# Kernel tuning notes

Measured on AMD Instinct MI355X. Metric: run time of the kernel, lower is better.

The kernel has to match this reference:

```python
import jax, jax.numpy as jnp
import numpy as np

HEADS = 16
DIM_HEAD = 64
LN_EPS = 1e-3  # keras LayerNormalization default


def setup_inputs() -> dict:
    key = jax.random.key(0)
    ks = jax.random.split(key, 4)
    B, N, D = 8, 512, 1024
    inner = HEADS * DIM_HEAD  # 1024
    return {
        "x": jax.random.normal(ks[0], (B, N, D), dtype=jnp.float32),
        "w_qkv": jax.random.normal(ks[1], (D, 3 * inner), dtype=jnp.float32) * (D ** -0.5),
        "reattn_w": jax.random.normal(ks[2], (HEADS, HEADS), dtype=jnp.float32),
        "ln_gamma": jnp.ones((HEADS,), dtype=jnp.float32),
        "ln_beta": jnp.zeros((HEADS,), dtype=jnp.float32),
        "w_out": jax.random.normal(ks[3], (inner, D), dtype=jnp.float32) * (inner ** -0.5),
        "b_out": jnp.zeros((D,), dtype=jnp.float32),
    }


def reference(x, w_qkv, reattn_w, ln_gamma, ln_beta, w_out, b_out):
    B, N, D = x.shape
    H, dh = HEADS, DIM_HEAD
    scale = dh ** -0.5

    qkv = x @ w_qkv  # [B, N, 3*H*dh]
    q, k, v = jnp.split(qkv, 3, axis=-1)
    # b n (h d) -> b h n d
    to_heads = lambda t: t.reshape(B, N, H, dh).transpose(0, 2, 1, 3)
    q, k, v = to_heads(q), to_heads(k), to_heads(v)

    dots = jnp.einsum("bhid,bhjd->bhij", q, k) * scale  # [B, H, N, N]
    attn = jax.nn.softmax(dots, axis=-1)

    # re-attention: mix across heads
    attn = jnp.einsum("bhij,hg->bgij", attn, reattn_w)

    # LayerNorm over the head axis (axis=1), keras default eps
    mean = jnp.mean(attn, axis=1, keepdims=True)
    var = jnp.var(attn, axis=1, keepdims=True)
    attn = (attn - mean) * jax.lax.rsqrt(var + LN_EPS)
    attn = attn * ln_gamma[None, :, None, None] + ln_beta[None, :, None, None]

    out = jnp.einsum("bhij,bhjd->bhid", attn, v)  # [B, H, N, dh]
    out = out.transpose(0, 2, 1, 3).reshape(B, N, H * dh)  # b h n d -> b n (h d)
    return out @ w_out + b_out
```

## Files before the change

kernel.cpp:

```cpp
#include <hip/hip_runtime.h>
#include <math.h>

#define BB 8
#define NN 512
#define DD 1024
#define HH 16
#define DH 64
#define INNER 1024
#define QKV3 3072
#define PSTR (NN * NN + 64)

typedef __attribute__((ext_vector_type(8))) short short8;
typedef __attribute__((ext_vector_type(4))) float f32x4;

#define AS1 __attribute__((address_space(1)))
#define AS3 __attribute__((address_space(3)))

__device__ __forceinline__ float4 ld4(const float* p) { return *(const float4*)p; }

__device__ __forceinline__ unsigned short f2bf(float f) {
    unsigned u = __float_as_uint(f);
    return (unsigned short)((u + 0x7fffu + ((u >> 16) & 1u)) >> 16);
}
__device__ __forceinline__ float bf2f(unsigned short u) {
    return __uint_as_float(((unsigned)u) << 16);
}

__global__ void preprocess(const float* __restrict__ x, unsigned short* __restrict__ xb,
                           const float* __restrict__ wq, unsigned short* __restrict__ wqT,
                           const float* __restrict__ wo, unsigned short* __restrict__ woT) {
    __shared__ float t[32][33];
    const int tid = threadIdx.x;
    const int bx = blockIdx.x;
    if (bx < 4096) {
        size_t i = ((size_t)bx * 256 + tid) * 4;
        float4 v = ld4(x + i);
        ushort4 o;
        o.x = f2bf(v.x); o.y = f2bf(v.y); o.z = f2bf(v.z); o.w = f2bf(v.w);
        *(ushort4*)(xb + i) = o;
        return;
    }
    const float* in; unsigned short* out; int K, N, n0, k0;
    if (bx < 7168) {
        const int bb = bx - 4096;
        in = wq; out = wqT; K = DD; N = QKV3;
        n0 = (bb % 96) * 32; k0 = (bb / 96) * 32;
    } else {
        const int bb = bx - 7168;
        in = wo; out = woT; K = INNER; N = INNER;
        n0 = (bb & 31) * 32; k0 = (bb >> 5) * 32;
    }
    const int tx = tid & 31, ty = tid >> 5;
#pragma unroll
    for (int l = 0; l < 4; ++l)
        t[ty + 8 * l][tx] = in[(size_t)(k0 + ty + 8 * l) * N + n0 + tx];
    __syncthreads();
#pragma unroll
    for (int l = 0; l < 4; ++l)
        out[(size_t)(n0 + ty + 8 * l) * K + k0 + tx] = f2bf(t[tx][ty + 8 * l]);
}

__device__ __forceinline__ void stage128(const unsigned short* __restrict__ A,
                                         const unsigned short* __restrict__ Bt,
                                         int K, int bm, int bn, int kt,
                                         short* sb, int w, int l) {
#pragma unroll
    for (int t = 0; t < 2; ++t) {
        const int q = w * 2 + t;
        const int li = q * 512 + l * 8;
        const int row = li >> 5, kc = li & 31;
        __builtin_amdgcn_global_load_lds(
            (const AS1 void*)(A + (size_t)(bm + row) * K + kt * 32 + kc),
            (AS3 void*)(sb + q * 512), 16, 0, 0);
        __builtin_amdgcn_global_load_lds(
            (const AS1 void*)(Bt + (size_t)(bn + row) * K + kt * 32 + kc),
            (AS3 void*)(sb + 4096 + q * 512), 16, 0, 0);
    }
}

__global__ __launch_bounds__(256) void gemm_bf16(
    const unsigned short* __restrict__ A, const unsigned short* __restrict__ Bt,
    float* __restrict__ C, const float* __restrict__ bias, int M, int N, int K) {
    __shared__ __align__(16) short lds_[2 * 8192];
    const int tid = threadIdx.x;
    const int w = tid >> 6, l = tid & 63;
    const int bm = blockIdx.y * 128, bn = blockIdx.x * 128;
    const int wm = (w >> 1) * 64, wn = (w & 1) * 64;
    const int lrow = l & 15, lq = l >> 4;
    const int NT = K >> 5;

    f32x4 acc[4][4];
#pragma unroll
    for (int i = 0; i < 4; ++i)
#pragma unroll
        for (int j = 0; j < 4; ++j) acc[i][j] = (f32x4){0.f, 0.f, 0.f, 0.f};

    stage128(A, Bt, K, bm, bn, 0, lds_, w, l);
    asm volatile("s_waitcnt vmcnt(0)" ::: "memory");
    __builtin_amdgcn_s_barrier();

    for (int t = 0; t < NT; ++t) {
        const int s = t & 1;
        if (t + 1 < NT)
            stage128(A, Bt, K, bm, bn, t + 1, lds_ + (s ^ 1) * 8192, w, l);
        const short* As_ = lds_ + s * 8192;
        const short* Bs_ = As_ + 4096;
        short8 a[4], b[4];
#pragma unroll
        for (int i = 0; i < 4; ++i)
            a[i] = *(const short8*)(As_ + (wm + i * 16 + lrow) * 32 + lq * 8);
#pragma unroll
        for (int j = 0; j < 4; ++j)
            b[j] = *(const short8*)(Bs_ + (wn + j * 16 + lrow) * 32 + lq * 8);

        asm volatile("s_waitcnt lgkmcnt(0)" ::: "memory");
        __builtin_amdgcn_sched_barrier(0);

        __builtin_amdgcn_s_setprio(1);
#pragma unroll
        for (int i = 0; i < 4; ++i)
#pragma unroll
            for (int j = 0; j < 4; ++j)
                acc[i][j] = __builtin_amdgcn_mfma_f32_16x16x32_bf16(a[i], b[j], acc[i][j], 0, 0, 0);
        __builtin_amdgcn_s_setprio(0);

        asm volatile("s_waitcnt vmcnt(0)" ::: "memory");
        __builtin_amdgcn_s_barrier();
    }

#pragma unroll
    for (int i = 0; i < 4; ++i)
#pragma unroll
        for (int j = 0; j < 4; ++j) {
            const int col = bn + wn + j * 16 + lrow;
            const float bv = bias ? bias[col] : 0.f;
#pragma unroll
            for (int r = 0; r < 4; ++r) {
                const int row = bm + wm + i * 16 + lq * 4 + r;
                C[(size_t)row * N + col] = acc[i][j][r] + bv;
            }
        }
}

__device__ __forceinline__ void stage_st(const unsigned short* __restrict__ G, int K,
                                         int row0, int kt, short* dst_half,
                                         int w, int l) {
    const int grow = row0 + w * 16 + (l >> 2);
    const int gcol = kt * 32 + (((l & 3) * 8) ^ ((l & 32) ? 16 : 0));
    __builtin_amdgcn_global_load_lds(
        (const AS1 void*)(G + (size_t)grow * K + gcol),
        (AS3 void*)(dst_half + w * 512), 16, 0, 0);
}

__global__ __launch_bounds__(512, 4) void gemm256_bf(
    const unsigned short* __restrict__ A, const unsigned short* __restrict__ Bt,
    unsigned short* __restrict__ C, int M, int N, int K) {
    __shared__ __align__(16) short lds_[2 * 12288];
    const int tid = threadIdx.x;
    const int w = tid >> 6, l = tid & 63;
    const int wmi = w >> 1, wni = w & 1;
    const int lrow = l & 15, lq = l >> 4;
    const int bm = blockIdx.y * 256, bn = blockIdx.x * 128;
    const int NT = K >> 5;

    const int aoff = lrow * 32 + ((lq * 8) ^ ((lrow & 8) ? 16 : 0));

    f32x4 acc[4][4];
#pragma unroll
    for (int i = 0; i < 4; ++i)
#pragma unroll
        for (int j = 0; j < 4; ++j) acc[i][j] = (f32x4){0.f, 0.f, 0.f, 0.f};

    stage_st(A,  K, bm,       0, lds_ + 0,    w, l);
    stage_st(A,  K, bm + 128, 0, lds_ + 4096, w, l);
    stage_st(Bt, K, bn,       0, lds_ + 8192, w, l);
    asm volatile("s_waitcnt vmcnt(0)" ::: "memory");
    __builtin_amdgcn_s_barrier();

    for (int t = 0; t < NT; ++t) {
        const int s = t & 1;
        if (t + 1 < NT) {
            short* nb = lds_ + (s ^ 1) * 12288;
            stage_st(A,  K, bm,       t + 1, nb,        w, l);
            stage_st(A,  K, bm + 128, t + 1, nb + 4096, w, l);
            stage_st(Bt, K, bn,       t + 1, nb + 8192, w, l);
        }
        const short* cb = lds_ + s * 12288;
        short8 a[4], b[4];
#pragma unroll
        for (int i = 0; i < 4; ++i)
            a[i] = *(const short8*)(cb + (wmi * 4 + i) * 512 + aoff);
#pragma unroll
        for (int j = 0; j < 4; ++j)
            b[j] = *(const short8*)(cb + 8192 + (wni * 4 + j) * 512 + aoff);

        asm volatile("s_waitcnt lgkmcnt(0)" ::: "memory");
        __builtin_amdgcn_sched_barrier(0);

        __builtin_amdgcn_s_setprio(1);
#pragma unroll
        for (int i = 0; i < 4; ++i)
#pragma unroll
            for (int j = 0; j < 4; ++j)
                acc[i][j] = __builtin_amdgcn_mfma_f32_16x16x32_bf16(a[i], b[j], acc[i][j], 0, 0, 0);
        __builtin_amdgcn_s_setprio(0);

        asm volatile("s_waitcnt vmcnt(0)" ::: "memory");
        __builtin_amdgcn_s_barrier();
    }

#pragma unroll
    for (int i = 0; i < 4; ++i)
#pragma unroll
        for (int j = 0; j < 4; ++j) {
            const int col = bn + wni * 64 + j * 16 + lrow;
#pragma unroll
            for (int r = 0; r < 4; ++r) {
                const int row = bm + wmi * 64 + i * 16 + lq * 4 + r;
                C[(size_t)row * N + col] = f2bf(acc[i][j][r]);
            }
        }
}

__global__ __launch_bounds__(256) void scores_tv(
    const unsigned short* __restrict__ qkvb, unsigned short* __restrict__ attnb,
    unsigned short* __restrict__ vT, float* __restrict__ lsum2) {
    __shared__ unsigned short sh[256 * 64 + 4 * 16 * 68];
    const int bx = blockIdx.x;
    const int tid = threadIdx.x;

    if (bx >= 2048) {
        const int t = bx - 2048;
        const int j0 = (t & 15) * 32;
        const int d0 = ((t >> 4) & 1) * 32;
        const int bh = t >> 5;
        const int h = bh & 15, b = bh >> 4;
        unsigned short (*tt)[33] = (unsigned short(*)[33])sh;
        const int tx = tid & 31, ty = tid >> 5;
        const unsigned short* src = qkvb + (size_t)(b * NN) * QKV3 + 2 * INNER + h * DH;
#pragma unroll
        for (int k = 0; k < 4; ++k)
            tt[ty + 8 * k][tx] = src[(size_t)(j0 + ty + 8 * k) * QKV3 + d0 + tx];
        __syncthreads();
        unsigned short* dst = vT + (size_t)bh * DH * NN;
#pragma unroll
        for (int k = 0; k < 4; ++k)
            dst[(size_t)(d0 + ty + 8 * k) * NN + j0 + tx] = tt[tx][ty + 8 * k];
        return;
    }

    unsigned short* Ks = sh;
    unsigned short* obuf = sh + 16384;
    const int bh = bx & 127;
    const int h = bh & 15, b = bh >> 4;
    const int jh = (bx >> 7) & 1;
    const int w = tid >> 6, l = tid & 63;
    const int i0 = (bx >> 8) * 64 + w * 16;
    const int lrow = l & 15, lq = l >> 4;

    const unsigned short* kbase =
        qkvb + (size_t)(b * NN + jh * 256) * QKV3 + INNER + h * DH;
#pragma unroll
    for (int i = 0; i < 8; ++i) {
        const int r = (w * 8 + i) * 8 + (l >> 3);
        const int c = (l & 7) ^ (r & 7);
        __builtin_amdgcn_global_load_lds(
            (const AS1 void*)(kbase + (size_t)r * QKV3 + c * 8),
            (AS3 void*)(Ks + (w * 8 + i) * 512), 16, 0, 0);
    }

    const unsigned short* qb = qkvb + (size_t)(b * NN) * QKV3 + h * DH + lq * 8;
    const short8 qf0 = *(const short8*)(qb + (size_t)(i0 + lrow) * QKV3);
    const short8 qf1 = *(const short8*)(qb + (size_t)(i0 + lrow) * QKV3 + 32);

    asm volatile("s_waitcnt vmcnt(0)" ::: "memory");
    __syncthreads();

    unsigned short* obase = attnb + (size_t)bh * PSTR + (size_t)i0 * NN + jh * 256;
    unsigned short* ob = obuf + (w * 16) * 68;
    const int sw = lrow & 7;
    float lacc = 0.f;
#pragma unroll
    for (int jt = 0; jt < 16; ++jt) {
        const int R = jt * 16 + lrow;
        const short8 kf0 = *(const short8*)(Ks + R * 64 + ((lq ^ sw) * 8));
        const short8 kf1 = *(const short8*)(Ks + R * 64 + (((4 + lq) ^ sw) * 8));
        f32x4 acc = (f32x4){0.f, 0.f, 0.f, 0.f};
        acc = __builtin_amdgcn_mfma_f32_16x16x32_bf16(kf0, qf0, acc, 0, 0, 0);
        acc = __builtin_amdgcn_mfma_f32_16x16x32_bf16(kf1, qf1, acc, 0, 0, 0);
        float e0 = __expf(acc[0] * 0.125f);
        float e1 = __expf(acc[1] * 0.125f);
        float e2 = __expf(acc[2] * 0.125f);
        float e3 = __expf(acc[3] * 0.125f);
        lacc += (e0 + e1) + (e2 + e3);
        ushort4 o;
        o.x = f2bf(e0); o.y = f2bf(e1); o.z = f2bf(e2); o.w = f2bf(e3);
        *(ushort4*)(ob + lrow * 68 + (jt & 3) * 16 + lq * 4) = o;
        if ((jt & 3) == 3) {
            const int jb = (jt >> 2) * 64;
#pragma unroll
            for (int q = 0; q < 4; ++q) {
                const int rr = q * 4 + (l >> 4);
                const int cc = l & 15;
                *(ushort4*)(obase + (size_t)rr * NN + jb + cc * 4) =
                    *(const ushort4*)(ob + rr * 68 + cc * 4);
            }
        }
    }
    lacc += __shfl_xor(lacc, 16, 64);
    lacc += __shfl_xor(lacc, 32, 64);
    if (lq == 0)
        lsum2[(size_t)jh * BB * HH * NN + (size_t)bh * NN + i0 + lrow] = lacc;
}

__global__ __launch_bounds__(512) void reattn_pv(
    const unsigned short* __restrict__ attnb, const unsigned short* __restrict__ vT,
    const float* __restrict__ lsum2, const float* __restrict__ rw,
    const float* __restrict__ gamma, const float* __restrict__ beta,
    unsigned short* __restrict__ outhb) {
    __shared__ unsigned short Ash[16 * 16 * 64];
    __shared__ float wsh[16][16];
    __shared__ float linv[16][16];
    __shared__ float gsh[16], bsh[16];

    const int b = blockIdx.x >> 5;
    const int i0 = (blockIdx.x & 31) * 16;
    const int tid = threadIdx.x;
    const int w = tid >> 6, l = tid & 63;
    const int lrow = l & 15, lq = l >> 4;

    if (tid < 256) {
        ((float*)wsh)[tid] = rw[tid];
        const int h = tid >> 4, i = tid & 15;
        const float s =
            lsum2[(size_t)(b * HH + h) * NN + i0 + i] +
            lsum2[(size_t)BB * HH * NN + (size_t)(b * HH + h) * NN + i0 + i];
        linv[h][i] = 1.0f / s;
    }
    if (tid < 16) { gsh[tid] = gamma[tid]; bsh[tid] = beta[tid]; }

    const int ri = w * 2 + (l >> 5);
    const int rj = (l & 31) * 2;
    const unsigned short* ebase =
        attnb + (size_t)(b * HH) * PSTR + (size_t)(i0 + ri) * NN + rj;

    f32x4 acc[2][4];
#pragma unroll
    for (int gg = 0; gg < 2; ++gg)
#pragma unroll
        for (int dt = 0; dt < 4; ++dt) acc[gg][dt] = (f32x4){0.f, 0.f, 0.f, 0.f};

    unsigned e[16];
#pragma unroll
    for (int h = 0; h < 16; ++h)
        e[h] = *(const unsigned*)(ebase + (size_t)h * PSTR);

    __syncthreads();

    const int g0 = w * 2;
    const int cch = rj >> 3;
    const int csw = ((cch ^ (ri & 7)) << 3) + (rj & 7);

    for (int jt = 0; jt < 8; ++jt) {
        float e0[16], e1[16];
#pragma unroll
        for (int h = 0; h < 16; ++h) {
            const float li = linv[h][ri];
            e0[h] = bf2f((unsigned short)(e[h] & 0xffffu)) * li;
            e1[h] = bf2f((unsigned short)(e[h] >> 16)) * li;
        }
        float m0[16], m1[16];
        float mean0 = 0.f, mean1 = 0.f;
#pragma unroll
        for (int g = 0; g < 16; ++g) {
            float s0 = 0.f, s1 = 0.f;
#pragma unroll
            for (int h = 0; h < 16; ++h) {
                const float wg = wsh[h][g];
                s0 += e0[h] * wg; s1 += e1[h] * wg;
            }
            m0[g] = s0; m1[g] = s1;
            mean0 += s0; mean1 += s1;
        }
        mean0 *= 0.0625f; mean1 *= 0.0625f;
        float va0 = 0.f, va1 = 0.f;
#pragma unroll
        for (int g = 0; g < 16; ++g) {
            const float d0 = m0[g] - mean0, d1 = m1[g] - mean1;
            va0 += d0 * d0; va1 += d1 * d1;
        }
        const float ri0 = rsqrtf(va0 * 0.0625f + 1e-3f);
        const float ri1 = rsqrtf(va1 * 0.0625f + 1e-3f);
#pragma unroll
        for (int g = 0; g < 16; ++g) {
            const unsigned short a0 = f2bf((m0[g] - mean0) * ri0 * gsh[g] + bsh[g]);
            const unsigned short a1 = f2bf((m1[g] - mean1) * ri1 * gsh[g] + bsh[g]);
            *(unsigned*)(&Ash[(g * 16 + ri) * 64 + csw]) = ((unsigned)a1 << 16) | (unsigned)a0;
        }
        __syncthreads();

        if (jt < 7) {
#pragma unroll
            for (int h = 0; h < 16; ++h)
                e[h] = *(const unsigned*)(ebase + (size_t)h * PSTR + (jt + 1) * 64);
        }
        const int j0 = jt * 64;
#pragma unroll
        for (int gg = 0; gg < 2; ++gg) {
            const int g = g0 + gg;
            const unsigned short* vb = vT + (size_t)(b * HH + g) * DH * NN;
#pragma unroll
            for (int kc = 0; kc < 2; ++kc) {
                const int cc = kc * 4 + lq;
                const short8 pf = *(const short8*)(
                    &Ash[(g * 16 + lrow) * 64 + ((cc ^ (lrow & 7)) << 3)]);
#pragma unroll
                for (int dt = 0; dt < 4; ++dt) {
                    const short8 vf = *(const short8*)(
                        vb + (size_t)(dt * 16 + lrow) * NN + j0 + kc * 32 + lq * 8);
                    acc[gg][dt] = __builtin_amdgcn_mfma_f32_16x16x32_bf16(
                        vf, pf, acc[gg][dt], 0, 0, 0);
                }
            }
        }
        __syncthreads();
    }

#pragma unroll
    for (int gg = 0; gg < 2; ++gg) {
        const int g = g0 + gg;
        unsigned short* orow = outhb +
            (size_t)(b * NN + i0 + lrow) * INNER + g * DH + lq * 4;
#pragma unroll
        for (int dt = 0; dt < 4; ++dt) {
            ushort4 o;
            o.x = f2bf(acc[gg][dt][0]); o.y = f2bf(acc[gg][dt][1]);
            o.z = f2bf(acc[gg][dt][2]); o.w = f2bf(acc[gg][dt][3]);
            *(ushort4*)(orow + dt * 16) = o;
        }
    }
}

extern "C" void kernel_launch(void* const* d_in, const int* in_sizes, int n_in,
                              void* d_out, int out_size, void* d_ws, size_t ws_size,
                              hipStream_t stream) {
    const float* x        = (const float*)d_in[0];
    const float* w_qkv    = (const float*)d_in[1];
    const float* reattn_w = (const float*)d_in[2];
    const float* ln_gamma = (const float*)d_in[3];
    const float* ln_beta  = (const float*)d_in[4];
    const float* w_out    = (const float*)d_in[5];
    const float* b_out    = (const float*)d_in[6];
    float* out = (float*)d_out;

    unsigned short* qkvb  = (unsigned short*)d_ws;
    unsigned short* attnb = qkvb + (size_t)BB * NN * QKV3;
    unsigned short* vTb   = attnb + (size_t)BB * HH * PSTR;
    unsigned short* outhb = vTb + (size_t)BB * HH * DH * NN;
    unsigned short* xb    = outhb + (size_t)BB * NN * INNER;
    unsigned short* wqkvT = xb + (size_t)BB * NN * DD;
    unsigned short* woutT = wqkvT + (size_t)DD * QKV3;
    float*          lsum2 = (float*)(woutT + (size_t)INNER * INNER);

    dim3 blk(256);

    preprocess<<<dim3(8192), blk, 0, stream>>>(x, xb, w_qkv, wqkvT, w_out, woutT);

    gemm256_bf<<<dim3(QKV3 / 128, (BB * NN) / 256), dim3(512), 0, stream>>>(
        xb, wqkvT, qkvb, BB * NN, QKV3, DD);

    scores_tv<<<dim3(6144), blk, 0, stream>>>(qkvb, attnb, vTb, lsum2);

    reattn_pv<<<dim3(BB * 32), dim3(512), 0, stream>>>(
        attnb, vTb, lsum2, reattn_w, ln_gamma, ln_beta, outhb);

    gemm_bf16<<<dim3(INNER / 128, (BB * NN) / 128), blk, 0, stream>>>(
        outhb, woutT, out, b_out, BB * NN, INNER, INNER);
}
```

Baseline: 222.8 us.

## Prefetch next attention tile earlier, batch V loads, and interleave batches across blocks

```diff
diff --git a/kernel.cpp b/kernel.cpp
--- a/kernel.cpp
+++ b/kernel.cpp
@@ -323,8 +323,8 @@
     __shared__ float linv[16][16];
     __shared__ float gsh[16], bsh[16];
 
-    const int b = blockIdx.x >> 5;
-    const int i0 = (blockIdx.x & 31) * 16;
+    const int b = blockIdx.x & 7;
+    const int i0 = (blockIdx.x >> 3) * 16;
     const int tid = threadIdx.x;
     const int w = tid >> 6, l = tid & 63;
     const int lrow = l & 15, lq = l >> 4;
@@ -350,10 +350,10 @@
 #pragma unroll
         for (int dt = 0; dt < 4; ++dt) acc[gg][dt] = (f32x4){0.f, 0.f, 0.f, 0.f};
 
-    unsigned e[16];
+    unsigned ecur[16];
 #pragma unroll
     for (int h = 0; h < 16; ++h)
-        e[h] = *(const unsigned*)(ebase + (size_t)h * PSTR);
+        ecur[h] = *(const unsigned*)(ebase + (size_t)h * PSTR);
 
     __syncthreads();
 
@@ -366,8 +366,14 @@
 #pragma unroll
         for (int h = 0; h < 16; ++h) {
             const float li = linv[h][ri];
-            e0[h] = bf2f((unsigned short)(e[h] & 0xffffu)) * li;
-            e1[h] = bf2f((unsigned short)(e[h] >> 16)) * li;
+            e0[h] = bf2f((unsigned short)(ecur[h] & 0xffffu)) * li;
+            e1[h] = bf2f((unsigned short)(ecur[h] >> 16)) * li;
+        }
+        unsigned enxt[16];
+        if (jt < 7) {
+#pragma unroll
+            for (int h = 0; h < 16; ++h)
+                enxt[h] = *(const unsigned*)(ebase + (size_t)h * PSTR + (jt + 1) * 64);
         }
         float m0[16], m1[16];
         float mean0 = 0.f, mean1 = 0.f;
@@ -399,31 +405,38 @@
         }
         __syncthreads();
 
-        if (jt < 7) {
-#pragma unroll
-            for (int h = 0; h < 16; ++h)
-                e[h] = *(const unsigned*)(ebase + (size_t)h * PSTR + (jt + 1) * 64);
-        }
         const int j0 = jt * 64;
+        short8 vfr[16];
+#pragma unroll
+        for (int gg = 0; gg < 2; ++gg) {
+            const unsigned short* vb = vT + (size_t)(b * HH + g0 + gg) * DH * NN;
+#pragma unroll
+            for (int kc = 0; kc < 2; ++kc)
+#pragma unroll
+                for (int dt = 0; dt < 4; ++dt)
+                    vfr[gg * 8 + kc * 4 + dt] = *(const short8*)(
+                        vb + (size_t)(dt * 16 + lrow) * NN + j0 + kc * 32 + lq * 8);
+        }
 #pragma unroll
         for (int gg = 0; gg < 2; ++gg) {
             const int g = g0 + gg;
-            const unsigned short* vb = vT + (size_t)(b * HH + g) * DH * NN;
 #pragma unroll
             for (int kc = 0; kc < 2; ++kc) {
                 const int cc = kc * 4 + lq;
                 const short8 pf = *(const short8*)(
                     &Ash[(g * 16 + lrow) * 64 + ((cc ^ (lrow & 7)) << 3)]);
 #pragma unroll
-                for (int dt = 0; dt < 4; ++dt) {
-                    const short8 vf = *(const short8*)(
-                        vb + (size_t)(dt * 16 + lrow) * NN + j0 + kc * 32 + lq * 8);
+                for (int dt = 0; dt < 4; ++dt)
                     acc[gg][dt] = __builtin_amdgcn_mfma_f32_16x16x32_bf16(
-                        vf, pf, acc[gg][dt], 0, 0, 0);
-                }
+                        vfr[gg * 8 + kc * 4 + dt], pf, acc[gg][dt], 0, 0, 0);
             }
         }
         __syncthreads();
+
+        if (jt < 7) {
+#pragma unroll
+            for (int h = 0; h < 16; ++h) ecur[h] = enxt[h];
+        }
     }
 
 #pragma unroll
```

New measurement: 219.5 us. Within noise of the previous version (-1.5%).
